# Performance work log

Hardware: AMD Instinct MI355X
Metric: run time of the kernel (lower is better)

Reference implementation:

```python
import jax, jax.numpy as jnp
import numpy as np

B, NC, N, DN, ALPHA = 8, 64, 128, 64, 2
HS, HM, HMOD = 256, 256, 64
STATE_IN, MSG_IN = 3 * DN, 2 * DN
MOD_IN = 2 * DN + 5
MOD_OUT = N * N + N


def _u(key, shape, fan_in):
    # kaiming_uniform-like init
    bound = 1.0 / np.sqrt(fan_in)
    return jax.random.uniform(key, shape, jnp.float32, -bound, bound)


def setup_inputs() -> dict:
    key = jax.random.key(0)
    ks = jax.random.split(key, 24)
    f = jnp.float32
    return {
        'h': jax.random.normal(ks[0], (B, NC, N, DN), f) * 0.01,
        'msg': jax.random.normal(ks[1], (B, NC, N, DN), f) * 0.01,
        'W': jax.random.normal(ks[2], (B, NC, N, N), f) * 0.05,
        'decay_logit': jnp.zeros((B, NC, N), f),
        'readout_drift': jnp.zeros((B, NC, 1), f),
        's_mem_live': jnp.zeros((B,), f),
        's_mem_ema_fast': jnp.zeros((B,), f),
        'H_aug_t': jax.random.normal(ks[3], (B, NC * DN), f),
        'neuron_id': jax.random.normal(ks[4], (NC, N, DN), f) * 0.02,
        'state_w1': _u(ks[5], (HS, STATE_IN), STATE_IN),
        'state_b1': jnp.zeros((HS,), f),
        'state_w2': _u(ks[6], (DN, HS), HS) * 0.1,
        'state_b2': jnp.zeros((DN,), f),
        'msg_w1': _u(ks[7], (HM, MSG_IN), MSG_IN),
        'msg_b1': jnp.zeros((HM,), f),
        'msg_w2': _u(ks[8], (DN, HM), HM) * 0.1,
        'msg_b2': jnp.zeros((DN,), f),
        'inject_w': _u(ks[9], (NC, ALPHA * DN, DN), DN),
        'inject_b': jnp.zeros((NC, ALPHA * DN), f),
        'mod_w1': _u(ks[10], (NC, MOD_IN, HMOD), HMOD),
        'mod_b1': jnp.zeros((NC, HMOD), f),
        'mod_w2': _u(ks[11], (NC, HMOD, MOD_OUT), MOD_OUT) * 0.01,
        'mod_b2': jnp.zeros((NC, MOD_OUT), f),
    }


def _mlp2(x, w1, b1, w2, b2):
    # F.linear -> tanh -> F.linear -> tanh
    hid = jnp.tanh(jnp.einsum('...i,hi->...h', x, w1) + b1)
    return jnp.tanh(jnp.einsum('...h,oh->...o', hid, w2) + b2)


def reference(h, msg, W, decay_logit, readout_drift, s_mem_live, s_mem_ema_fast,
              H_aug_t, neuron_id, state_w1, state_b1, state_w2, state_b2,
              msg_w1, msg_b1, msg_w2, msg_b2, inject_w, inject_b,
              mod_w1, mod_b1, mod_w2, mod_b2):
    # --- message passing: received = W @ msg  [B,NC,N,DN] ---
    received = jnp.einsum('bcij,bcjd->bcid', W, msg)

    # --- inject external input into the first ALPHA (input) neurons ---
    cell_slice = H_aug_t.reshape(B, NC, DN)               # [B,NC,DN]
    inject = jnp.einsum('bni,noi->bno', cell_slice, inject_w) + inject_b[None]
    inject = inject.reshape(B, NC, ALPHA, DN)
    received = received.at[:, :, :ALPHA].add(inject)

    # --- state update MLP (shared across cells/neurons) ---
    nid = jnp.broadcast_to(neuron_id[None], (B, NC, N, DN))
    state_in = jnp.concatenate([h, received, nid], axis=-1)      # [B,NC,N,3*DN]
    h_new = _mlp2(state_in, state_w1, state_b1, state_w2, state_b2)

    # --- message MLP ---
    msg_in = jnp.concatenate([h_new, received], axis=-1)         # [B,NC,N,2*DN]
    msg_new = _mlp2(msg_in, msg_w1, msg_b1, msg_w2, msg_b2)

    # --- modulator input (per _build_mod_input) ---
    h_mean = h_new.mean(axis=2)                                  # [B,NC,DN]
    msg_mean = msg_new.mean(axis=2)                              # [B,NC,DN]
    W_stats = jnp.abs(W).mean(axis=-1).mean(axis=2, keepdims=True)  # [B,NC,1]
    decay_mean = decay_logit.mean(axis=2, keepdims=True)         # [B,NC,1]
    s1 = jnp.broadcast_to(s_mem_live[:, None, None], (B, NC, 1))
    s2 = jnp.broadcast_to(s_mem_ema_fast[:, None, None], (B, NC, 1))
    mod_input = jnp.concatenate(
        [h_mean, msg_mean, W_stats, decay_mean, readout_drift, s1, s2], axis=-1)

    # --- per-cell modulator MLP (per _modulator_forward) ---
    hidden = jnp.tanh(jnp.einsum('bni,nih->bnh', mod_input, mod_w1) + mod_b1[None])
    mod_out = jnp.einsum('bnh,nho->bno', hidden, mod_w2) + mod_b2[None]

    # --- apply modulator action to recurrent adjacency + decay ---
    delta_W = mod_out[..., :N * N].reshape(B, NC, N, N)
    delta_decay = mod_out[..., N * N:N * N + N].reshape(B, NC, N)
    W_new = W + delta_W
    decay_new = decay_logit + delta_decay
    return (h_new, msg_new, W_new, decay_new)
```

## Files before the change

### kernel.cpp

```cpp
#include <hip/hip_runtime.h>
#include <hip/hip_bf16.h>
#include <math.h>


typedef __bf16 bf16_t;
typedef __attribute__((ext_vector_type(8))) __bf16 bf16x8;
typedef __attribute__((ext_vector_type(4))) float f32x4;

__device__ __forceinline__ float fast_tanh(float x) {
  float e = __expf(2.0f * x);
  return 1.0f - 2.0f / (e + 1.0f);
}

__device__ __forceinline__ f32x4 mfma16(bf16x8 a, bf16x8 b, f32x4 c) {
  return __builtin_amdgcn_mfma_f32_16x16x32_bf16(a, b, c, 0, 0, 0);
}

__global__ __launch_bounds__(256) void k_convert(
    const float* __restrict__ sw1, const float* __restrict__ sw2,
    const float* __restrict__ mw1, const float* __restrict__ mw2,
    bf16_t* __restrict__ out) {
  int i = blockIdx.x * 256 + threadIdx.x;
  float v;
  if (i < 49152) v = sw1[i];
  else if (i < 65536) v = sw2[i - 49152];
  else if (i < 98304) v = mw1[i - 65536];
  else v = mw2[i - 98304];
  out[i] = (bf16_t)v;
}

__global__ __launch_bounds__(256) void k_received(
    const float* __restrict__ W, const float* __restrict__ msg,
    const float* __restrict__ Haug, const float* __restrict__ injw,
    const float* __restrict__ injb, float* __restrict__ rec,
    float* __restrict__ wstats) {
  int bc = blockIdx.x, c = bc & 63, b = bc >> 6;
  __shared__ bf16_t Wt[128][136];
  __shared__ bf16_t Mt[64][136];
  __shared__ float inj[128];
  __shared__ float red[256];
  int t = threadIdx.x;
  const float* Wp = W + (size_t)bc * 16384;
  float asum = 0.f;
  for (int s = 0; s < 16; ++s) {
    int e = (s * 256 + t) * 4;
    f32x4 v = *(const f32x4*)(Wp + e);
    int i = e >> 7, j = e & 127;
#pragma unroll
    for (int u = 0; u < 4; ++u) { Wt[i][j + u] = (bf16_t)v[u]; asum += fabsf(v[u]); }
  }
  const float* Mp = msg + (size_t)bc * 8192;
  for (int s = 0; s < 8; ++s) {
    int e = (s * 256 + t) * 4;
    f32x4 v = *(const f32x4*)(Mp + e);
    int j = e >> 6, d = e & 63;
#pragma unroll
    for (int u = 0; u < 4; ++u) Mt[d + u][j] = (bf16_t)v[u];
  }
  if (t < 128) {
    const float* cell = Haug + (size_t)b * 4096 + c * 64;
    const float* iw = injw + (size_t)c * 8192 + t * 64;
    float a = injb[c * 128 + t];
    for (int k = 0; k < 64; ++k) a += cell[k] * iw[k];
    inj[t] = a;
  }
  red[t] = asum;
  __syncthreads();
  for (int s = 128; s > 0; s >>= 1) {
    if (t < s) red[t] += red[t + s];
    __syncthreads();
  }
  if (t == 0) wstats[bc] = red[0];

  int wave = t >> 6, l = t & 63, lr = l & 15, kg = l >> 4;
  f32x4 acc[2][4] = {};
#pragma unroll
  for (int ks = 0; ks < 4; ++ks) {
    int kof = ks * 32 + kg * 8;
    bf16x8 a0 = *(const bf16x8*)&Wt[wave * 32 + lr][kof];
    bf16x8 a1 = *(const bf16x8*)&Wt[wave * 32 + 16 + lr][kof];
#pragma unroll
    for (int ni = 0; ni < 4; ++ni) {
      bf16x8 bfr = *(const bf16x8*)&Mt[ni * 16 + lr][kof];
      acc[0][ni] = mfma16(a0, bfr, acc[0][ni]);
      acc[1][ni] = mfma16(a1, bfr, acc[1][ni]);
    }
  }
  float* rp = rec + (size_t)bc * 8192;
#pragma unroll
  for (int mi = 0; mi < 2; ++mi)
#pragma unroll
    for (int ni = 0; ni < 4; ++ni)
#pragma unroll
      for (int r = 0; r < 4; ++r) {
        int row = wave * 32 + mi * 16 + kg * 4 + r, col = ni * 16 + lr;
        float v = acc[mi][ni][r];
        if (row < 2) v += inj[row * 64 + col];
        rp[row * 64 + col] = v;
      }
}

__global__ __launch_bounds__(256) void k_mlp(
    const float* __restrict__ h, const float* __restrict__ rec,
    const float* __restrict__ nid, const bf16_t* __restrict__ wbf,
    const float* __restrict__ sb1, const float* __restrict__ sb2,
    const float* __restrict__ msb1, const float* __restrict__ msb2,
    float* __restrict__ out_h, float* __restrict__ out_m) {
  int blk = blockIdx.x;
  int bc = blk >> 1, c = bc & 63, half = blk & 1;
  __shared__ bf16_t xs[64][200];
  __shared__ bf16_t wc[64][200];
  __shared__ bf16_t hs[64][72];
  int t = threadIdx.x;
  size_t rowbase = (size_t)bc * 8192 + (size_t)half * 4096;
  const float* hp = h + rowbase;
  const float* rp = rec + rowbase;
  const float* np2 = nid + (size_t)c * 8192 + (size_t)half * 4096;
  for (int s = 0; s < 4; ++s) {
    int e = (s * 256 + t) * 4;
    int row = e >> 6, col = e & 63;
    f32x4 v1 = *(const f32x4*)(hp + e);
    f32x4 v2 = *(const f32x4*)(rp + e);
    f32x4 v3 = *(const f32x4*)(np2 + e);
#pragma unroll
    for (int j = 0; j < 4; ++j) {
      xs[row][col + j] = (bf16_t)v1[j];
      xs[row][64 + col + j] = (bf16_t)v2[j];
      xs[row][128 + col + j] = (bf16_t)v3[j];
    }
  }
  int wave = t >> 6, l = t & 63, lr = l & 15, kg = l >> 4;
  const bf16_t* w1b = wbf;
  const bf16_t* w2b = wbf + 49152;
  const bf16_t* w3b = wbf + 65536;
  const bf16_t* w4b = wbf + 98304;

  f32x4 acc2[4] = {};
  for (int hc = 0; hc < 4; ++hc) {
    __syncthreads();
    for (int s = 0; s < 6; ++s) {
      int e = (s * 256 + t) * 8;
      int hh = e / 192, kk = e % 192;
      *(bf16x8*)&wc[hh][kk] = *(const bf16x8*)(w1b + (size_t)(hc * 64 + hh) * 192 + kk);
    }
    __syncthreads();
    f32x4 a1[4] = {};
#pragma unroll
    for (int ks = 0; ks < 6; ++ks) {
      int kof = ks * 32 + kg * 8;
      bf16x8 af = *(const bf16x8*)&xs[wave * 16 + lr][kof];
#pragma unroll
      for (int ni = 0; ni < 4; ++ni) {
        bf16x8 bfr = *(const bf16x8*)&wc[ni * 16 + lr][kof];
        a1[ni] = mfma16(af, bfr, a1[ni]);
      }
    }
#pragma unroll
    for (int ni = 0; ni < 4; ++ni) {
      float bias = sb1[hc * 64 + ni * 16 + lr];
#pragma unroll
      for (int r = 0; r < 4; ++r)
        hs[wave * 16 + kg * 4 + r][ni * 16 + lr] = (bf16_t)fast_tanh(a1[ni][r] + bias);
    }
#pragma unroll
    for (int ks = 0; ks < 2; ++ks) {
      int kof = ks * 32 + kg * 8;
      bf16x8 af = *(const bf16x8*)&hs[wave * 16 + lr][kof];
#pragma unroll
      for (int ni = 0; ni < 4; ++ni) {
        bf16x8 bfr = *(const bf16x8*)(w2b + (size_t)(ni * 16 + lr) * 256 + hc * 64 + kof);
        acc2[ni] = mfma16(af, bfr, acc2[ni]);
      }
    }
  }
  float* ohp = out_h + rowbase;
#pragma unroll
  for (int ni = 0; ni < 4; ++ni) {
    float bias = sb2[ni * 16 + lr];
#pragma unroll
    for (int r = 0; r < 4; ++r) {
      int row = wave * 16 + kg * 4 + r, col = ni * 16 + lr;
      float v = fast_tanh(acc2[ni][r] + bias);
      ohp[row * 64 + col] = v;
      hs[row][col] = (bf16_t)v;
    }
  }

  f32x4 acc3[4] = {};
  for (int hc = 0; hc < 4; ++hc) {
    __syncthreads();
    for (int s = 0; s < 4; ++s) {
      int e = (s * 256 + t) * 8;
      int hh = e >> 7, kk = e & 127;
      *(bf16x8*)&wc[hh][kk] = *(const bf16x8*)(w3b + (size_t)(hc * 64 + hh) * 128 + kk);
    }
    __syncthreads();
    f32x4 g3[4] = {};
#pragma unroll
    for (int ks = 0; ks < 4; ++ks) {
      int kof = ks * 32 + kg * 8;
      bf16x8 af;
      if (ks < 2) af = *(const bf16x8*)&hs[wave * 16 + lr][kof];
      else        af = *(const bf16x8*)&xs[wave * 16 + lr][kof];
#pragma unroll
      for (int ni = 0; ni < 4; ++ni) {
        bf16x8 bfr = *(const bf16x8*)&wc[ni * 16 + lr][kof];
        g3[ni] = mfma16(af, bfr, g3[ni]);
      }
    }
#pragma unroll
    for (int ni = 0; ni < 4; ++ni) {
      float bias = msb1[hc * 64 + ni * 16 + lr];
#pragma unroll
      for (int r = 0; r < 4; ++r)
        xs[wave * 16 + kg * 4 + r][128 + ni * 16 + lr] = (bf16_t)fast_tanh(g3[ni][r] + bias);
    }
#pragma unroll
    for (int ks = 0; ks < 2; ++ks) {
      int kof = ks * 32 + kg * 8;
      bf16x8 af = *(const bf16x8*)&xs[wave * 16 + lr][128 + kof];
#pragma unroll
      for (int ni = 0; ni < 4; ++ni) {
        bf16x8 bfr = *(const bf16x8*)(w4b + (size_t)(ni * 16 + lr) * 256 + hc * 64 + kof);
        acc3[ni] = mfma16(af, bfr, acc3[ni]);
      }
    }
  }
  float* omp = out_m + rowbase;
#pragma unroll
  for (int ni = 0; ni < 4; ++ni) {
    float bias = msb2[ni * 16 + lr];
#pragma unroll
    for (int r = 0; r < 4; ++r) {
      int row = wave * 16 + kg * 4 + r, col = ni * 16 + lr;
      omp[row * 64 + col] = fast_tanh(acc3[ni][r] + bias);
    }
  }
}

__global__ __launch_bounds__(256) void k_mod(
    const float* __restrict__ out_h, const float* __restrict__ out_m,
    const float* __restrict__ decay, const float* __restrict__ rdrift,
    const float* __restrict__ sml, const float* __restrict__ smf,
    const float* __restrict__ wstats, const float* __restrict__ mw1,
    const float* __restrict__ mb1, float* __restrict__ hidden) {
  int bc = blockIdx.x, c = bc & 63, b = bc >> 6;
  __shared__ float red[256];
  __shared__ float modin[133];
  int t = threadIdx.x, d = t & 63, q = t >> 6;
  const float* hp = out_h + (size_t)bc * 8192;
  const float* mp = out_m + (size_t)bc * 8192;
  float s1 = 0.f, s2 = 0.f;
  for (int i = q * 32; i < q * 32 + 32; ++i) { s1 += hp[i * 64 + d]; s2 += mp[i * 64 + d]; }
  red[t] = s1; __syncthreads();
  if (q == 0) modin[d] = (red[d] + red[64 + d] + red[128 + d] + red[192 + d]) * (1.f / 128.f);
  __syncthreads();
  red[t] = s2; __syncthreads();
  if (q == 0) modin[64 + d] = (red[d] + red[64 + d] + red[128 + d] + red[192 + d]) * (1.f / 128.f);
  __syncthreads();
  red[t] = (t < 128) ? decay[(size_t)bc * 128 + t] : 0.f;
  __syncthreads();
  if (t == 0) {
    float s = 0.f;
    for (int i = 0; i < 128; ++i) s += red[i];
    modin[128] = wstats[bc] * (1.f / 16384.f);
    modin[129] = s * (1.f / 128.f);
    modin[130] = rdrift[bc];
    modin[131] = sml[b];
    modin[132] = smf[b];
  }
  __syncthreads();
  if (t < 64) {
    const float* w = mw1 + (size_t)c * 133 * 64;
    float a = mb1[c * 64 + t];
    for (int i = 0; i < 133; ++i) a += modin[i] * w[i * 64 + t];
    hidden[(size_t)bc * 64 + t] = fast_tanh(a);
  }
}

__global__ __launch_bounds__(256) void k_apply(
    const float* __restrict__ hidden, const float* __restrict__ mw2,
    const float* __restrict__ mb2, const float* __restrict__ W,
    const float* __restrict__ decay, float* __restrict__ out_W,
    float* __restrict__ out_d) {
  int c = blockIdx.y, ch = blockIdx.x, t = threadIdx.x;
  __shared__ float hid[8][64];
  int b0 = t >> 6, h0 = t & 63;
  hid[b0][h0] = hidden[(size_t)(b0 * 64 + c) * 64 + h0];
  hid[b0 + 4][h0] = hidden[(size_t)((b0 + 4) * 64 + c) * 64 + h0];
  __syncthreads();
  int o = ch * 1024 + t * 4;
  if (o >= 16512) return;
  const float* w2 = mw2 + (size_t)c * 64 * 16512 + o;
  f32x4 bias = *(const f32x4*)(mb2 + (size_t)c * 16512 + o);
  f32x4 acc[8];
#pragma unroll
  for (int b = 0; b < 8; ++b) acc[b] = bias;
  for (int hh = 0; hh < 64; ++hh) {
    f32x4 wv = *(const f32x4*)(w2 + (size_t)hh * 16512);
#pragma unroll
    for (int b = 0; b < 8; ++b) acc[b] += hid[b][hh] * wv;
  }
  if (o < 16384) {
#pragma unroll
    for (int b = 0; b < 8; ++b) {
      size_t idx = (size_t)(b * 64 + c) * 16384 + o;
      f32x4 wv = *(const f32x4*)(W + idx);
      *(f32x4*)(out_W + idx) = wv + acc[b];
    }
  } else {
    int i = o - 16384;
#pragma unroll
    for (int b = 0; b < 8; ++b) {
      size_t idx = (size_t)(b * 64 + c) * 128 + i;
      f32x4 dv = *(const f32x4*)(decay + idx);
      *(f32x4*)(out_d + idx) = dv + acc[b];
    }
  }
}

extern "C" void kernel_launch(void* const* d_in, const int* in_sizes, int n_in,
                              void* d_out, int out_size, void* d_ws, size_t ws_size,
                              hipStream_t stream) {
  const float* h = (const float*)d_in[0];
  const float* msg = (const float*)d_in[1];
  const float* W = (const float*)d_in[2];
  const float* decay = (const float*)d_in[3];
  const float* rdrift = (const float*)d_in[4];
  const float* sml = (const float*)d_in[5];
  const float* smf = (const float*)d_in[6];
  const float* Haug = (const float*)d_in[7];
  const float* nid = (const float*)d_in[8];
  const float* sw1 = (const float*)d_in[9];
  const float* sb1 = (const float*)d_in[10];
  const float* sw2 = (const float*)d_in[11];
  const float* sb2 = (const float*)d_in[12];
  const float* mw1 = (const float*)d_in[13];
  const float* mb1 = (const float*)d_in[14];
  const float* mw2 = (const float*)d_in[15];
  const float* mb2 = (const float*)d_in[16];
  const float* injw = (const float*)d_in[17];
  const float* injb = (const float*)d_in[18];
  const float* modw1 = (const float*)d_in[19];
  const float* modb1 = (const float*)d_in[20];
  const float* modw2 = (const float*)d_in[21];
  const float* modb2 = (const float*)d_in[22];

  float* out = (float*)d_out;
  float* out_h = out;
  float* out_m = out + 4194304;
  float* out_W = out + 8388608;
  float* out_d = out + 16777216;

  char* wsb = (char*)d_ws;
  float* rec = (float*)wsb;
  float* wstats = (float*)(wsb + 16777216);
  float* hidden = (float*)(wsb + 16777216 + 4096);
  bf16_t* wbf = (bf16_t*)(wsb + 16777216 + 4096 + 131072);

  k_convert<<<448, 256, 0, stream>>>(sw1, sw2, mw1, mw2, wbf);
  k_received<<<512, 256, 0, stream>>>(W, msg, Haug, injw, injb, rec, wstats);
  k_mlp<<<1024, 256, 0, stream>>>(h, rec, nid, wbf, sb1, sb2, mb1, mb2, out_h, out_m);
  k_mod<<<512, 256, 0, stream>>>(out_h, out_m, decay, rdrift, sml, smf, wstats,
                                 modw1, modb1, hidden);
  k_apply<<<dim3(17, 64), 256, 0, stream>>>(hidden, modw2, modb2, W, decay, out_W, out_d);
}
```

Baseline: 552.3 us.

## Fuse received matmul with MLPs, pre-convert inputs to bf16, stream apply stores

Merges k_received and k_mlp into a single per-cell kernel. The received tensor stays in shared memory as bf16 instead of round-tripping through global fp32, and weight fragments are read straight from global instead of being staged through LDS with barriers. A new prep kernel converts W, h and neuron_id to bf16 and computes the W abs-sum statistics up front. k_apply now reads a transposed hidden layout directly, with no shared memory or barrier, and uses nontemporal loads and stores. k_mod's decay sum becomes a tree reduction. The cost is an extra full bf16 copy of W, h and nid written and reread through the workspace, and higher register pressure from the 2x fragment tiling.

Result: no change. 554.2 us (+0.4%).

```diff
diff --git a/kernel.cpp b/kernel.cpp
--- a/kernel.cpp
+++ b/kernel.cpp
@@ -4,6 +4,7 @@
 
 
 typedef __bf16 bf16_t;
+typedef __attribute__((ext_vector_type(4))) __bf16 bf16x4;
 typedef __attribute__((ext_vector_type(8))) __bf16 bf16x8;
 typedef __attribute__((ext_vector_type(4))) float f32x4;
 
@@ -16,39 +17,74 @@
   return __builtin_amdgcn_mfma_f32_16x16x32_bf16(a, b, c, 0, 0, 0);
 }
 
-__global__ __launch_bounds__(256) void k_convert(
-    const float* __restrict__ sw1, const float* __restrict__ sw2,
-    const float* __restrict__ mw1, const float* __restrict__ mw2,
-    bf16_t* __restrict__ out) {
-  int i = blockIdx.x * 256 + threadIdx.x;
-  float v;
-  if (i < 49152) v = sw1[i];
-  else if (i < 65536) v = sw2[i - 49152];
-  else if (i < 98304) v = mw1[i - 65536];
-  else v = mw2[i - 98304];
-  out[i] = (bf16_t)v;
-}
-
-__global__ __launch_bounds__(256) void k_received(
-    const float* __restrict__ W, const float* __restrict__ msg,
+__global__ __launch_bounds__(256) void k_prep(
+    const float* __restrict__ W, const float* __restrict__ h,
+    const float* __restrict__ nid, const float* __restrict__ sw1,
+    const float* __restrict__ sw2, const float* __restrict__ mw1,
+    const float* __restrict__ mw2, bf16_t* __restrict__ Wbf,
+    bf16_t* __restrict__ hbf, bf16_t* __restrict__ nidbf,
+    bf16_t* __restrict__ wbf, float* __restrict__ wstats) {
+  int blk = blockIdx.x, t = threadIdx.x;
+  if (blk < 512) {
+    __shared__ float red[256];
+    const float* Wp = W + (size_t)blk * 16384;
+    bf16_t* op = Wbf + (size_t)blk * 16384;
+    float asum = 0.f;
+    for (int s = 0; s < 16; ++s) {
+      int e = (s * 256 + t) * 4;
+      f32x4 v = *(const f32x4*)(Wp + e);
+      bf16x4 o;
+#pragma unroll
+      for (int u = 0; u < 4; ++u) { o[u] = (bf16_t)v[u]; asum += fabsf(v[u]); }
+      *(bf16x4*)(op + e) = o;
+    }
+    red[t] = asum;
+    __syncthreads();
+    for (int s = 128; s > 0; s >>= 1) {
+      if (t < s) red[t] += red[t + s];
+      __syncthreads();
+    }
+    if (t == 0) wstats[blk] = red[0];
+  } else if (blk < 2816) {
+    int g = (blk - 512) * 2048 + t * 8;
+    const float* src;
+    bf16_t* dst;
+    int off;
+    if (g < 4194304) { src = h; dst = hbf; off = g; }
+    else { src = nid; dst = nidbf; off = g - 4194304; }
+    f32x4 v0 = *(const f32x4*)(src + off);
+    f32x4 v1 = *(const f32x4*)(src + off + 4);
+    bf16x8 o;
+#pragma unroll
+    for (int u = 0; u < 4; ++u) { o[u] = (bf16_t)v0[u]; o[u + 4] = (bf16_t)v1[u]; }
+    *(bf16x8*)(dst + off) = o;
+  } else {
+    int i = (blk - 2816) * 256 + t;
+    float v;
+    if (i < 49152) v = sw1[i];
+    else if (i < 65536) v = sw2[i - 49152];
+    else if (i < 98304) v = mw1[i - 65536];
+    else v = mw2[i - 98304];
+    wbf[i] = (bf16_t)v;
+  }
+}
+
+__global__ __launch_bounds__(256) void k_fused(
+    const bf16_t* __restrict__ Wbf, const float* __restrict__ msg,
+    const bf16_t* __restrict__ hbf, const bf16_t* __restrict__ nidbf,
     const float* __restrict__ Haug, const float* __restrict__ injw,
-    const float* __restrict__ injb, float* __restrict__ rec,
-    float* __restrict__ wstats) {
+    const float* __restrict__ injb, const bf16_t* __restrict__ wbf,
+    const float* __restrict__ sb1, const float* __restrict__ sb2,
+    const float* __restrict__ msb1, const float* __restrict__ msb2,
+    float* __restrict__ out_h, float* __restrict__ out_m) {
   int bc = blockIdx.x, c = bc & 63, b = bc >> 6;
-  __shared__ bf16_t Wt[128][136];
   __shared__ bf16_t Mt[64][136];
+  __shared__ bf16_t recs[128][72];
+  __shared__ bf16_t hs[128][72];
+  __shared__ bf16_t hnew[128][72];
   __shared__ float inj[128];
-  __shared__ float red[256];
   int t = threadIdx.x;
-  const float* Wp = W + (size_t)bc * 16384;
-  float asum = 0.f;
-  for (int s = 0; s < 16; ++s) {
-    int e = (s * 256 + t) * 4;
-    f32x4 v = *(const f32x4*)(Wp + e);
-    int i = e >> 7, j = e & 127;
-#pragma unroll
-    for (int u = 0; u < 4; ++u) { Wt[i][j + u] = (bf16_t)v[u]; asum += fabsf(v[u]); }
-  }
+
   const float* Mp = msg + (size_t)bc * 8192;
   for (int s = 0; s < 8; ++s) {
     int e = (s * 256 + t) * 4;
@@ -64,178 +100,163 @@
     for (int k = 0; k < 64; ++k) a += cell[k] * iw[k];
     inj[t] = a;
   }
-  red[t] = asum;
-  __syncthreads();
-  for (int s = 128; s > 0; s >>= 1) {
-    if (t < s) red[t] += red[t + s];
-    __syncthreads();
-  }
-  if (t == 0) wstats[bc] = red[0];
+  __syncthreads();
 
   int wave = t >> 6, l = t & 63, lr = l & 15, kg = l >> 4;
-  f32x4 acc[2][4] = {};
+  int r0 = wave * 32;
+
+  const bf16_t* Wp = Wbf + (size_t)bc * 16384;
+  f32x4 racc[2][4] = {};
 #pragma unroll
   for (int ks = 0; ks < 4; ++ks) {
     int kof = ks * 32 + kg * 8;
-    bf16x8 a0 = *(const bf16x8*)&Wt[wave * 32 + lr][kof];
-    bf16x8 a1 = *(const bf16x8*)&Wt[wave * 32 + 16 + lr][kof];
+    bf16x8 a0 = *(const bf16x8*)(Wp + (size_t)(r0 + lr) * 128 + kof);
+    bf16x8 a1 = *(const bf16x8*)(Wp + (size_t)(r0 + 16 + lr) * 128 + kof);
 #pragma unroll
     for (int ni = 0; ni < 4; ++ni) {
       bf16x8 bfr = *(const bf16x8*)&Mt[ni * 16 + lr][kof];
-      acc[0][ni] = mfma16(a0, bfr, acc[0][ni]);
-      acc[1][ni] = mfma16(a1, bfr, acc[1][ni]);
-    }
-  }
-  float* rp = rec + (size_t)bc * 8192;
+      racc[0][ni] = mfma16(a0, bfr, racc[0][ni]);
+      racc[1][ni] = mfma16(a1, bfr, racc[1][ni]);
+    }
+  }
 #pragma unroll
   for (int mi = 0; mi < 2; ++mi)
 #pragma unroll
     for (int ni = 0; ni < 4; ++ni)
 #pragma unroll
       for (int r = 0; r < 4; ++r) {
-        int row = wave * 32 + mi * 16 + kg * 4 + r, col = ni * 16 + lr;
-        float v = acc[mi][ni][r];
+        int row = r0 + mi * 16 + kg * 4 + r, col = ni * 16 + lr;
+        float v = racc[mi][ni][r];
         if (row < 2) v += inj[row * 64 + col];
-        rp[row * 64 + col] = v;
-      }
-}
-
-__global__ __launch_bounds__(256) void k_mlp(
-    const float* __restrict__ h, const float* __restrict__ rec,
-    const float* __restrict__ nid, const bf16_t* __restrict__ wbf,
-    const float* __restrict__ sb1, const float* __restrict__ sb2,
-    const float* __restrict__ msb1, const float* __restrict__ msb2,
-    float* __restrict__ out_h, float* __restrict__ out_m) {
-  int blk = blockIdx.x;
-  int bc = blk >> 1, c = bc & 63, half = blk & 1;
-  __shared__ bf16_t xs[64][200];
-  __shared__ bf16_t wc[64][200];
-  __shared__ bf16_t hs[64][72];
-  int t = threadIdx.x;
-  size_t rowbase = (size_t)bc * 8192 + (size_t)half * 4096;
-  const float* hp = h + rowbase;
-  const float* rp = rec + rowbase;
-  const float* np2 = nid + (size_t)c * 8192 + (size_t)half * 4096;
-  for (int s = 0; s < 4; ++s) {
-    int e = (s * 256 + t) * 4;
-    int row = e >> 6, col = e & 63;
-    f32x4 v1 = *(const f32x4*)(hp + e);
-    f32x4 v2 = *(const f32x4*)(rp + e);
-    f32x4 v3 = *(const f32x4*)(np2 + e);
-#pragma unroll
-    for (int j = 0; j < 4; ++j) {
-      xs[row][col + j] = (bf16_t)v1[j];
-      xs[row][64 + col + j] = (bf16_t)v2[j];
-      xs[row][128 + col + j] = (bf16_t)v3[j];
-    }
-  }
-  int wave = t >> 6, l = t & 63, lr = l & 15, kg = l >> 4;
+        recs[row][col] = (bf16_t)v;
+      }
+
+  const bf16_t* hp = hbf + (size_t)bc * 8192;
+  const bf16_t* np2 = nidbf + (size_t)c * 8192;
+  bf16x8 aA[2][6];
+#pragma unroll
+  for (int mi = 0; mi < 2; ++mi) {
+    int row = r0 + mi * 16 + lr;
+#pragma unroll
+    for (int ks = 0; ks < 6; ++ks) {
+      int kof = ks * 32 + kg * 8;
+      if (ks < 2)      aA[mi][ks] = *(const bf16x8*)(hp + (size_t)row * 64 + kof);
+      else if (ks < 4) aA[mi][ks] = *(const bf16x8*)&recs[row][kof - 64];
+      else             aA[mi][ks] = *(const bf16x8*)(np2 + (size_t)row * 64 + (kof - 128));
+    }
+  }
   const bf16_t* w1b = wbf;
   const bf16_t* w2b = wbf + 49152;
   const bf16_t* w3b = wbf + 65536;
   const bf16_t* w4b = wbf + 98304;
-
-  f32x4 acc2[4] = {};
+  f32x4 acc2[2][4] = {};
   for (int hc = 0; hc < 4; ++hc) {
-    __syncthreads();
-    for (int s = 0; s < 6; ++s) {
-      int e = (s * 256 + t) * 8;
-      int hh = e / 192, kk = e % 192;
-      *(bf16x8*)&wc[hh][kk] = *(const bf16x8*)(w1b + (size_t)(hc * 64 + hh) * 192 + kk);
-    }
-    __syncthreads();
-    f32x4 a1[4] = {};
+    f32x4 a1[2][4] = {};
 #pragma unroll
     for (int ks = 0; ks < 6; ++ks) {
       int kof = ks * 32 + kg * 8;
-      bf16x8 af = *(const bf16x8*)&xs[wave * 16 + lr][kof];
-#pragma unroll
-      for (int ni = 0; ni < 4; ++ni) {
-        bf16x8 bfr = *(const bf16x8*)&wc[ni * 16 + lr][kof];
-        a1[ni] = mfma16(af, bfr, a1[ni]);
-      }
-    }
+#pragma unroll
+      for (int ni = 0; ni < 4; ++ni) {
+        bf16x8 bfr = *(const bf16x8*)(w1b + (size_t)(hc * 64 + ni * 16 + lr) * 192 + kof);
+        a1[0][ni] = mfma16(aA[0][ks], bfr, a1[0][ni]);
+        a1[1][ni] = mfma16(aA[1][ks], bfr, a1[1][ni]);
+      }
+    }
+#pragma unroll
+    for (int mi = 0; mi < 2; ++mi)
+#pragma unroll
+      for (int ni = 0; ni < 4; ++ni) {
+        float bias = sb1[hc * 64 + ni * 16 + lr];
+#pragma unroll
+        for (int r = 0; r < 4; ++r)
+          hs[r0 + mi * 16 + kg * 4 + r][ni * 16 + lr] = (bf16_t)fast_tanh(a1[mi][ni][r] + bias);
+      }
+#pragma unroll
+    for (int ks = 0; ks < 2; ++ks) {
+      int kof = ks * 32 + kg * 8;
+      bf16x8 af0 = *(const bf16x8*)&hs[r0 + lr][kof];
+      bf16x8 af1 = *(const bf16x8*)&hs[r0 + 16 + lr][kof];
+#pragma unroll
+      for (int ni = 0; ni < 4; ++ni) {
+        bf16x8 bfr = *(const bf16x8*)(w2b + (size_t)(ni * 16 + lr) * 256 + hc * 64 + kof);
+        acc2[0][ni] = mfma16(af0, bfr, acc2[0][ni]);
+        acc2[1][ni] = mfma16(af1, bfr, acc2[1][ni]);
+      }
+    }
+  }
+  float* ohp = out_h + (size_t)bc * 8192;
+#pragma unroll
+  for (int mi = 0; mi < 2; ++mi)
 #pragma unroll
     for (int ni = 0; ni < 4; ++ni) {
-      float bias = sb1[hc * 64 + ni * 16 + lr];
-#pragma unroll
-      for (int r = 0; r < 4; ++r)
-        hs[wave * 16 + kg * 4 + r][ni * 16 + lr] = (bf16_t)fast_tanh(a1[ni][r] + bias);
-    }
+      float bias = sb2[ni * 16 + lr];
+#pragma unroll
+      for (int r = 0; r < 4; ++r) {
+        int row = r0 + mi * 16 + kg * 4 + r, col = ni * 16 + lr;
+        float v = fast_tanh(acc2[mi][ni][r] + bias);
+        ohp[row * 64 + col] = v;
+        hnew[row][col] = (bf16_t)v;
+      }
+    }
+
+  bf16x8 aB[2][4];
+#pragma unroll
+  for (int mi = 0; mi < 2; ++mi) {
+    int row = r0 + mi * 16 + lr;
+#pragma unroll
+    for (int ks = 0; ks < 4; ++ks) {
+      int kof = ks * 32 + kg * 8;
+      if (ks < 2) aB[mi][ks] = *(const bf16x8*)&hnew[row][kof];
+      else        aB[mi][ks] = *(const bf16x8*)&recs[row][kof - 64];
+    }
+  }
+  f32x4 acc3[2][4] = {};
+  for (int hc = 0; hc < 4; ++hc) {
+    f32x4 g3[2][4] = {};
+#pragma unroll
+    for (int ks = 0; ks < 4; ++ks) {
+      int kof = ks * 32 + kg * 8;
+#pragma unroll
+      for (int ni = 0; ni < 4; ++ni) {
+        bf16x8 bfr = *(const bf16x8*)(w3b + (size_t)(hc * 64 + ni * 16 + lr) * 128 + kof);
+        g3[0][ni] = mfma16(aB[0][ks], bfr, g3[0][ni]);
+        g3[1][ni] = mfma16(aB[1][ks], bfr, g3[1][ni]);
+      }
+    }
+#pragma unroll
+    for (int mi = 0; mi < 2; ++mi)
+#pragma unroll
+      for (int ni = 0; ni < 4; ++ni) {
+        float bias = msb1[hc * 64 + ni * 16 + lr];
+#pragma unroll
+        for (int r = 0; r < 4; ++r)
+          hs[r0 + mi * 16 + kg * 4 + r][ni * 16 + lr] = (bf16_t)fast_tanh(g3[mi][ni][r] + bias);
+      }
 #pragma unroll
     for (int ks = 0; ks < 2; ++ks) {
       int kof = ks * 32 + kg * 8;
-      bf16x8 af = *(const bf16x8*)&hs[wave * 16 + lr][kof];
-#pragma unroll
-      for (int ni = 0; ni < 4; ++ni) {
-        bf16x8 bfr = *(const bf16x8*)(w2b + (size_t)(ni * 16 + lr) * 256 + hc * 64 + kof);
-        acc2[ni] = mfma16(af, bfr, acc2[ni]);
-      }
-    }
-  }
-  float* ohp = out_h + rowbase;
-#pragma unroll
-  for (int ni = 0; ni < 4; ++ni) {
-    float bias = sb2[ni * 16 + lr];
-#pragma unroll
-    for (int r = 0; r < 4; ++r) {
-      int row = wave * 16 + kg * 4 + r, col = ni * 16 + lr;
-      float v = fast_tanh(acc2[ni][r] + bias);
-      ohp[row * 64 + col] = v;
-      hs[row][col] = (bf16_t)v;
-    }
-  }
-
-  f32x4 acc3[4] = {};
-  for (int hc = 0; hc < 4; ++hc) {
-    __syncthreads();
-    for (int s = 0; s < 4; ++s) {
-      int e = (s * 256 + t) * 8;
-      int hh = e >> 7, kk = e & 127;
-      *(bf16x8*)&wc[hh][kk] = *(const bf16x8*)(w3b + (size_t)(hc * 64 + hh) * 128 + kk);
-    }
-    __syncthreads();
-    f32x4 g3[4] = {};
-#pragma unroll
-    for (int ks = 0; ks < 4; ++ks) {
-      int kof = ks * 32 + kg * 8;
-      bf16x8 af;
-      if (ks < 2) af = *(const bf16x8*)&hs[wave * 16 + lr][kof];
-      else        af = *(const bf16x8*)&xs[wave * 16 + lr][kof];
-#pragma unroll
-      for (int ni = 0; ni < 4; ++ni) {
-        bf16x8 bfr = *(const bf16x8*)&wc[ni * 16 + lr][kof];
-        g3[ni] = mfma16(af, bfr, g3[ni]);
-      }
-    }
+      bf16x8 af0 = *(const bf16x8*)&hs[r0 + lr][kof];
+      bf16x8 af1 = *(const bf16x8*)&hs[r0 + 16 + lr][kof];
+#pragma unroll
+      for (int ni = 0; ni < 4; ++ni) {
+        bf16x8 bfr = *(const bf16x8*)(w4b + (size_t)(ni * 16 + lr) * 256 + hc * 64 + kof);
+        acc3[0][ni] = mfma16(af0, bfr, acc3[0][ni]);
+        acc3[1][ni] = mfma16(af1, bfr, acc3[1][ni]);
+      }
+    }
+  }
+  float* omp = out_m + (size_t)bc * 8192;
+#pragma unroll
+  for (int mi = 0; mi < 2; ++mi)
 #pragma unroll
     for (int ni = 0; ni < 4; ++ni) {
-      float bias = msb1[hc * 64 + ni * 16 + lr];
-#pragma unroll
-      for (int r = 0; r < 4; ++r)
-        xs[wave * 16 + kg * 4 + r][128 + ni * 16 + lr] = (bf16_t)fast_tanh(g3[ni][r] + bias);
-    }
-#pragma unroll
-    for (int ks = 0; ks < 2; ++ks) {
-      int kof = ks * 32 + kg * 8;
-      bf16x8 af = *(const bf16x8*)&xs[wave * 16 + lr][128 + kof];
-#pragma unroll
-      for (int ni = 0; ni < 4; ++ni) {
-        bf16x8 bfr = *(const bf16x8*)(w4b + (size_t)(ni * 16 + lr) * 256 + hc * 64 + kof);
-        acc3[ni] = mfma16(af, bfr, acc3[ni]);
-      }
-    }
-  }
-  float* omp = out_m + rowbase;
-#pragma unroll
-  for (int ni = 0; ni < 4; ++ni) {
-    float bias = msb2[ni * 16 + lr];
-#pragma unroll
-    for (int r = 0; r < 4; ++r) {
-      int row = wave * 16 + kg * 4 + r, col = ni * 16 + lr;
-      omp[row * 64 + col] = fast_tanh(acc3[ni][r] + bias);
-    }
-  }
+      float bias = msb2[ni * 16 + lr];
+#pragma unroll
+      for (int r = 0; r < 4; ++r) {
+        int row = r0 + mi * 16 + kg * 4 + r, col = ni * 16 + lr;
+        omp[row * 64 + col] = fast_tanh(acc3[mi][ni][r] + bias);
+      }
+    }
 }
 
 __global__ __launch_bounds__(256) void k_mod(
@@ -260,11 +281,13 @@
   __syncthreads();
   red[t] = (t < 128) ? decay[(size_t)bc * 128 + t] : 0.f;
   __syncthreads();
+  for (int s = 128; s > 0; s >>= 1) {
+    if (t < s) red[t] += red[t + s];
+    __syncthreads();
+  }
   if (t == 0) {
-    float s = 0.f;
-    for (int i = 0; i < 128; ++i) s += red[i];
     modin[128] = wstats[bc] * (1.f / 16384.f);
-    modin[129] = s * (1.f / 128.f);
+    modin[129] = red[0] * (1.f / 128.f);
     modin[130] = rdrift[bc];
     modin[131] = sml[b];
     modin[132] = smf[b];
@@ -274,7 +297,7 @@
     const float* w = mw1 + (size_t)c * 133 * 64;
     float a = mb1[c * 64 + t];
     for (int i = 0; i < 133; ++i) a += modin[i] * w[i * 64 + t];
-    hidden[(size_t)bc * 64 + t] = fast_tanh(a);
+    hidden[((size_t)(c * 64 + t)) * 8 + b] = fast_tanh(a);
   }
 }
 
@@ -284,29 +307,27 @@
     const float* __restrict__ decay, float* __restrict__ out_W,
     float* __restrict__ out_d) {
   int c = blockIdx.y, ch = blockIdx.x, t = threadIdx.x;
-  __shared__ float hid[8][64];
-  int b0 = t >> 6, h0 = t & 63;
-  hid[b0][h0] = hidden[(size_t)(b0 * 64 + c) * 64 + h0];
-  hid[b0 + 4][h0] = hidden[(size_t)((b0 + 4) * 64 + c) * 64 + h0];
-  __syncthreads();
   int o = ch * 1024 + t * 4;
   if (o >= 16512) return;
   const float* w2 = mw2 + (size_t)c * 64 * 16512 + o;
+  const float* hq = hidden + (size_t)c * 512;
   f32x4 bias = *(const f32x4*)(mb2 + (size_t)c * 16512 + o);
   f32x4 acc[8];
 #pragma unroll
   for (int b = 0; b < 8; ++b) acc[b] = bias;
   for (int hh = 0; hh < 64; ++hh) {
-    f32x4 wv = *(const f32x4*)(w2 + (size_t)hh * 16512);
-#pragma unroll
-    for (int b = 0; b < 8; ++b) acc[b] += hid[b][hh] * wv;
+    f32x4 wv = __builtin_nontemporal_load((const f32x4*)(w2 + (size_t)hh * 16512));
+    f32x4 h0 = *(const f32x4*)(hq + hh * 8);
+    f32x4 h1 = *(const f32x4*)(hq + hh * 8 + 4);
+#pragma unroll
+    for (int b = 0; b < 4; ++b) { acc[b] += h0[b] * wv; acc[b + 4] += h1[b] * wv; }
   }
   if (o < 16384) {
 #pragma unroll
     for (int b = 0; b < 8; ++b) {
       size_t idx = (size_t)(b * 64 + c) * 16384 + o;
       f32x4 wv = *(const f32x4*)(W + idx);
-      *(f32x4*)(out_W + idx) = wv + acc[b];
+      __builtin_nontemporal_store(wv + acc[b], (f32x4*)(out_W + idx));
     }
   } else {
     int i = o - 16384;
@@ -314,7 +335,7 @@
     for (int b = 0; b < 8; ++b) {
       size_t idx = (size_t)(b * 64 + c) * 128 + i;
       f32x4 dv = *(const f32x4*)(decay + idx);
-      *(f32x4*)(out_d + idx) = dv + acc[b];
+      __builtin_nontemporal_store(dv + acc[b], (f32x4*)(out_d + idx));
     }
   }
 }
@@ -353,14 +374,17 @@
   float* out_d = out + 16777216;
 
   char* wsb = (char*)d_ws;
-  float* rec = (float*)wsb;
-  float* wstats = (float*)(wsb + 16777216);
-  float* hidden = (float*)(wsb + 16777216 + 4096);
-  bf16_t* wbf = (bf16_t*)(wsb + 16777216 + 4096 + 131072);
-
-  k_convert<<<448, 256, 0, stream>>>(sw1, sw2, mw1, mw2, wbf);
-  k_received<<<512, 256, 0, stream>>>(W, msg, Haug, injw, injb, rec, wstats);
-  k_mlp<<<1024, 256, 0, stream>>>(h, rec, nid, wbf, sb1, sb2, mb1, mb2, out_h, out_m);
+  float* wstats = (float*)wsb;
+  float* hidden = (float*)(wsb + 4096);
+  bf16_t* wbf = (bf16_t*)(wsb + 4096 + 131072);
+  bf16_t* Wbf = (bf16_t*)(wsb + 524288);
+  bf16_t* hbf = (bf16_t*)(wsb + 524288 + 16777216);
+  bf16_t* nidbf = (bf16_t*)(wsb + 524288 + 16777216 + 8388608);
+
+  k_prep<<<3264, 256, 0, stream>>>(W, h, nid, sw1, sw2, mw1, mw2,
+                                   Wbf, hbf, nidbf, wbf, wstats);
+  k_fused<<<512, 256, 0, stream>>>(Wbf, msg, hbf, nidbf, Haug, injw, injb, wbf,
+                                   sb1, sb2, mb1, mb2, out_h, out_m);
   k_mod<<<512, 256, 0, stream>>>(out_h, out_m, decay, rdrift, sml, smf, wstats,
                                  modw1, modb1, hidden);
   k_apply<<<dim3(17, 64), 256, 0, stream>>>(hidden, modw2, modb2, W, decay, out_W, out_d);
```
